# Optimization experiments

Measured on AMD Instinct MI355X. Metric: run time of the kernel, lower is better.

Reference implementation:

```python
import jax, jax.numpy as jnp
import numpy as np

B, L, D = 64, 1024, 64  # (batch*heads, seq_len, head_dim)


def setup_inputs() -> dict:
    key = jax.random.key(0)
    kq, kk, kv = jax.random.split(key, 3)
    q = jax.random.normal(kq, (B, L, D), dtype=jnp.float32)
    k = jax.random.normal(kk, (B, L, D), dtype=jnp.float32)
    v = jax.random.normal(kv, (B, L, D), dtype=jnp.float32)
    scale = jnp.float32(1.0 / np.sqrt(D))  # standard 1/sqrt(d_head)
    return {"q": q, "k": k, "v": v, "scale": scale}


def reference(q, k, v, scale):
    # attention = bmm(q, k^T) * scale  -> [B, L, L]
    attention = jnp.einsum("bqd,bkd->bqk", q, k) * scale
    # softmax over dim=2 (keys); dropout p=0.0 is identity
    attention = jax.nn.softmax(attention, axis=2)
    # context = bmm(attention, v) -> [B, L, D]
    context = jnp.einsum("bqk,bkd->bqd", attention, v)
    return (context, attention)
```

## Files before the change

### kernel.cpp

```cpp
#include <hip/hip_runtime.h>
#include <hip/hip_bf16.h>

typedef __bf16 bf16x8 __attribute__((ext_vector_type(8)));
typedef __bf16 bf16x4 __attribute__((ext_vector_type(4)));
typedef float  f32x4  __attribute__((ext_vector_type(4)));

#define NB 64
#define LL 1024
#define DD 64
#define PB 40

#define WS_VT_OFF 0
#define WS_KB_OFF ((size_t)8 * 1024 * 1024)
#define WS_NEED   ((size_t)16 * 1024 * 1024)

#if __has_builtin(__builtin_amdgcn_exp2f)
#define EXP2(x) __builtin_amdgcn_exp2f(x)
#else
#define EXP2(x) exp2f(x)
#endif

__global__ __launch_bounds__(256)
void preconvert_kv(const float* __restrict__ k, const float* __restrict__ v,
                   __bf16* __restrict__ kbf, __bf16* __restrict__ vt) {
  const int blk = blockIdx.x, tid = threadIdx.x;
  if (blk < NB * (LL / 64)) {
    const int b = blk >> 4, t = blk & 15;
    __shared__ float tile[64][65];
    const float* src = v + ((size_t)b * LL + t * 64) * DD;
    for (int i = tid; i < 64 * 16; i += 256) {
      const int row = i >> 4, c4 = (i & 15) * 4;
      f32x4 x = *(const f32x4*)(src + row * DD + c4);
      tile[row][c4 + 0] = x[0]; tile[row][c4 + 1] = x[1];
      tile[row][c4 + 2] = x[2]; tile[row][c4 + 3] = x[3];
    }
    __syncthreads();
    __bf16* dst = vt + (size_t)b * DD * LL + t * 64;
    for (int i = tid; i < 64 * 8; i += 256) {
      const int d = i >> 3, k8 = (i & 7) * 8;
      bf16x8 o;
      #pragma unroll
      for (int j = 0; j < 8; ++j) o[j] = (__bf16)tile[k8 + j][d];
      *(bf16x8*)(dst + (size_t)d * LL + k8) = o;
    }
  } else {
    const size_t base = ((size_t)(blk - 1024) * 256 + tid) * 8;
    const f32x4* s = (const f32x4*)(k + base);
    f32x4 x0 = s[0], x1 = s[1];
    bf16x8 o;
    #pragma unroll
    for (int j = 0; j < 4; ++j) { o[j] = (__bf16)x0[j]; o[4 + j] = (__bf16)x1[j]; }
    *(bf16x8*)(kbf + base) = o;
  }
}

__global__ __launch_bounds__(256, 4)
void sdpa_quarter(const float* __restrict__ q, const __bf16* __restrict__ kbf,
                  const __bf16* __restrict__ vt, const float* __restrict__ scale_p,
                  float* __restrict__ out) {
  __shared__ __bf16 Kq[256 * 64];
  __shared__ __bf16 Pw[4 * 16 * PB];

  const int tid  = threadIdx.x;
  const int lane = tid & 63;
  const int w    = tid >> 6;
  const int l15  = lane & 15;
  const int lg   = lane >> 4;

  int bid = blockIdx.x;
  bid = (bid & 7) * 128 + (bid >> 3);
  const int b     = bid >> 4;
  const int qrow0 = (bid & 15) * 64 + w * 16;

  const float scale2 = scale_p[0] * 1.4426950408889634f;
  const __bf16* kb = kbf + (size_t)b * LL * DD;
  const __bf16* vb = vt  + (size_t)b * DD * LL;
  float* ctxb  = out + ((size_t)b * LL + qrow0) * DD;
  float* attnb = out + (size_t)NB * LL * DD + (size_t)b * LL * LL
               + (size_t)qrow0 * LL;

  bf16x8 aq[2];
  {
    const float* qrow = q + ((size_t)b * LL + qrow0 + l15) * DD;
    #pragma unroll
    for (int s = 0; s < 2; ++s) {
      const f32x4* p4 = (const f32x4*)(qrow + s * 32 + lg * 8);
      f32x4 x0 = p4[0], x1 = p4[1];
      #pragma unroll
      for (int j = 0; j < 4; ++j) {
        aq[s][j]     = (__bf16)(x0[j] * scale2);
        aq[s][4 + j] = (__bf16)(x1[j] * scale2);
      }
    }
  }

  const int xsw = (l15 & 7) * 8;
  __bf16* prow = Pw + (w * 16 + l15) * PB;

  float ls = 0.f;
  for (int qt = 0; qt < 4; ++qt) {
    __syncthreads();
    #pragma unroll
    for (int it = 0; it < 8; ++it) {
      const int c = it * 256 + tid;
      const int row = c >> 3, slot = c & 7;
      bf16x8 t = *(const bf16x8*)(kb + (size_t)(qt * 256 + row) * 64 + slot * 8);
      *(bf16x8*)(Kq + row * 64 + ((slot * 8) ^ ((row & 7) * 8))) = t;
    }
    __syncthreads();
    for (int kt = 0; kt < 8; ++kt) {
      bf16x8 bk[2][2];
      #pragma unroll
      for (int f = 0; f < 2; ++f)
        #pragma unroll
        for (int s = 0; s < 2; ++s)
          bk[f][s] = *(const bf16x8*)(Kq + (kt * 32 + f * 16 + l15) * 64
                                         + ((s * 32 + lg * 8) ^ xsw));
      f32x4 sacc[2] = {{0.f,0.f,0.f,0.f},{0.f,0.f,0.f,0.f}};
      #pragma unroll
      for (int s = 0; s < 2; ++s)
        #pragma unroll
        for (int f = 0; f < 2; ++f)
          sacc[f] = __builtin_amdgcn_mfma_f32_16x16x32_bf16(bk[f][s], aq[s], sacc[f], 0, 0, 0);
      #pragma unroll
      for (int f = 0; f < 2; ++f)
        #pragma unroll
        for (int r = 0; r < 4; ++r)
          ls += EXP2(sacc[f][r]);
    }
  }
  ls += __shfl_xor(ls, 16, 64);
  ls += __shfl_xor(ls, 32, 64);
  const float rl = 1.0f / ls;

  f32x4 cacc[4];
  #pragma unroll
  for (int g = 0; g < 4; ++g) cacc[g] = (f32x4){0.f, 0.f, 0.f, 0.f};

  for (int qt = 0; qt < 4; ++qt) {
    __syncthreads();
    #pragma unroll
    for (int it = 0; it < 8; ++it) {
      const int c = it * 256 + tid;
      const int row = c >> 3, slot = c & 7;
      bf16x8 t = *(const bf16x8*)(kb + (size_t)(qt * 256 + row) * 64 + slot * 8);
      *(bf16x8*)(Kq + row * 64 + ((slot * 8) ^ ((row & 7) * 8))) = t;
    }
    __syncthreads();

    for (int kt = 0; kt < 8; ++kt) {
      bf16x8 bv[4];
      #pragma unroll
      for (int g = 0; g < 4; ++g)
        bv[g] = *(const bf16x8*)(vb + (size_t)(g * 16 + l15) * LL
                                    + qt * 256 + kt * 32 + lg * 8);

      bf16x8 bk[2][2];
      #pragma unroll
      for (int f = 0; f < 2; ++f)
        #pragma unroll
        for (int s = 0; s < 2; ++s)
          bk[f][s] = *(const bf16x8*)(Kq + (kt * 32 + f * 16 + l15) * 64
                                         + ((s * 32 + lg * 8) ^ xsw));

      f32x4 sacc[2] = {{0.f,0.f,0.f,0.f},{0.f,0.f,0.f,0.f}};
      #pragma unroll
      for (int s = 0; s < 2; ++s)
        #pragma unroll
        for (int f = 0; f < 2; ++f)
          sacc[f] = __builtin_amdgcn_mfma_f32_16x16x32_bf16(bk[f][s], aq[s], sacc[f], 0, 0, 0);

      f32x4 pv[2];
      #pragma unroll
      for (int f = 0; f < 2; ++f)
        #pragma unroll
        for (int r = 0; r < 4; ++r)
          pv[f][r] = EXP2(sacc[f][r]) * rl;

      float* arow = attnb + (size_t)l15 * LL + qt * 256 + kt * 32 + lg * 4;
      *(f32x4*)(arow)      = pv[0];
      *(f32x4*)(arow + 16) = pv[1];

      #pragma unroll
      for (int f = 0; f < 2; ++f) {
        bf16x4 pb;
        #pragma unroll
        for (int r = 0; r < 4; ++r) pb[r] = (__bf16)pv[f][r];
        *(bf16x4*)(prow + f * 16 + lg * 4) = pb;
      }
      bf16x8 pa = *(const bf16x8*)(prow + lg * 8);
      #pragma unroll
      for (int g = 0; g < 4; ++g)
        cacc[g] = __builtin_amdgcn_mfma_f32_16x16x32_bf16(pa, bv[g], cacc[g], 0, 0, 0);
    }
  }

  #pragma unroll
  for (int g = 0; g < 4; ++g)
    #pragma unroll
    for (int r = 0; r < 4; ++r)
      ctxb[(size_t)(lg * 4 + r) * DD + g * 16 + l15] = cacc[g][r];
}

#define BQ 64
#define BK 32
#define KSTRIDE 72
#define VSTRIDE 40
#define PSTRIDE 48

__global__ __launch_bounds__(256, 4)
void sdpa_fallback(const float* __restrict__ q, const float* __restrict__ k,
                   const float* __restrict__ v, const float* __restrict__ scale_p,
                   float* __restrict__ out) {
  const int tid  = threadIdx.x;
  const int lane = tid & 63;
  const int w    = tid >> 6;
  int bid = blockIdx.x;
  bid = (bid & 7) * 128 + (bid >> 3);
  const int b    = bid >> 4;
  const int qblk = (bid & 15) * BQ;

  __shared__ __bf16 Ks[BK * KSTRIDE];
  __shared__ __bf16 Vs[DD * VSTRIDE];
  __shared__ __bf16 Pp[4][16 * PSTRIDE];

  const float scale = scale_p[0];
  const float* qb = q + ((size_t)b * LL + qblk) * DD;
  const float* kb = k + (size_t)b * LL * DD;
  const float* vb = v + (size_t)b * LL * DD;
  float* ctx  = out + ((size_t)b * LL + qblk) * DD;
  float* attn = out + (size_t)NB * LL * DD + (size_t)b * LL * LL + (size_t)qblk * LL;

  const int l15 = lane & 15;
  const int lg  = lane >> 4;
  const int dchunk = lg * 8;

  bf16x8 aq[2];
  {
    const float* qrow = qb + (size_t)(w * 16 + l15) * DD;
    #pragma unroll
    for (int s = 0; s < 2; ++s) {
      const f32x4* p4 = (const f32x4*)(qrow + s * 32 + dchunk);
      f32x4 x0 = p4[0], x1 = p4[1];
      #pragma unroll
      for (int j = 0; j < 4; ++j) {
        aq[s][j]     = (__bf16)(x0[j] * scale);
        aq[s][4 + j] = (__bf16)(x1[j] * scale);
      }
    }
  }

  const int srow = tid >> 3;
  const int sd0  = (tid & 7) * 8;

  float lpart[4] = {0.f, 0.f, 0.f, 0.f};
  for (int kt = 0; kt < LL / BK; ++kt) {
    __syncthreads();
    {
      const f32x4* src = (const f32x4*)(kb + (size_t)(kt * BK + srow) * DD + sd0);
      f32x4 x0 = src[0], x1 = src[1];
      bf16x8 t;
      #pragma unroll
      for (int j = 0; j < 4; ++j) { t[j] = (__bf16)x0[j]; t[4 + j] = (__bf16)x1[j]; }
      *(bf16x8*)&Ks[srow * KSTRIDE + sd0] = t;
    }
    __syncthreads();
    f32x4 sacc[2] = {{0.f,0.f,0.f,0.f},{0.f,0.f,0.f,0.f}};
    #pragma unroll
    for (int s = 0; s < 2; ++s)
      #pragma unroll
      for (int f = 0; f < 2; ++f) {
        bf16x8 bk = *(const bf16x8*)&Ks[(f * 16 + l15) * KSTRIDE + s * 32 + dchunk];
        sacc[f] = __builtin_amdgcn_mfma_f32_16x16x32_bf16(aq[s], bk, sacc[f], 0, 0, 0);
      }
    #pragma unroll
    for (int f = 0; f < 2; ++f)
      #pragma unroll
      for (int r = 0; r < 4; ++r)
        lpart[r] += __expf(sacc[f][r]);
  }
  #pragma unroll
  for (int m = 1; m < 16; m <<= 1)
    #pragma unroll
    for (int r = 0; r < 4; ++r)
      lpart[r] += __shfl_xor(lpart[r], m, 64);
  float rl[4];
  #pragma unroll
  for (int r = 0; r < 4; ++r) rl[r] = 1.0f / lpart[r];

  f32x4 cacc[4] = {{0.f,0.f,0.f,0.f},{0.f,0.f,0.f,0.f},
                   {0.f,0.f,0.f,0.f},{0.f,0.f,0.f,0.f}};
  for (int kt = 0; kt < LL / BK; ++kt) {
    __syncthreads();
    {
      const f32x4* src = (const f32x4*)(kb + (size_t)(kt * BK + srow) * DD + sd0);
      f32x4 x0 = src[0], x1 = src[1];
      bf16x8 t;
      #pragma unroll
      for (int j = 0; j < 4; ++j) { t[j] = (__bf16)x0[j]; t[4 + j] = (__bf16)x1[j]; }
      *(bf16x8*)&Ks[srow * KSTRIDE + sd0] = t;
      const f32x4* vsrc = (const f32x4*)(vb + (size_t)(kt * BK + srow) * DD + sd0);
      f32x4 y0 = vsrc[0], y1 = vsrc[1];
      #pragma unroll
      for (int j = 0; j < 4; ++j) {
        Vs[(sd0 + j)     * VSTRIDE + srow] = (__bf16)y0[j];
        Vs[(sd0 + 4 + j) * VSTRIDE + srow] = (__bf16)y1[j];
      }
    }
    __syncthreads();
    f32x4 sacc[2] = {{0.f,0.f,0.f,0.f},{0.f,0.f,0.f,0.f}};
    #pragma unroll
    for (int s = 0; s < 2; ++s)
      #pragma unroll
      for (int f = 0; f < 2; ++f) {
        bf16x8 bk = *(const bf16x8*)&Ks[(f * 16 + l15) * KSTRIDE + s * 32 + dchunk];
        sacc[f] = __builtin_amdgcn_mfma_f32_16x16x32_bf16(aq[s], bk, sacc[f], 0, 0, 0);
      }
    #pragma unroll
    for (int f = 0; f < 2; ++f)
      #pragma unroll
      for (int r = 0; r < 4; ++r) {
        const int row = lg * 4 + r;
        float p = __expf(sacc[f][r]) * rl[r];
        attn[(size_t)(w * 16 + row) * LL + (kt * BK + f * 16 + l15)] = p;
        Pp[w][row * PSTRIDE + f * 16 + l15] = (__bf16)p;
      }
    bf16x8 pa = *(const bf16x8*)&Pp[w][l15 * PSTRIDE + lg * 8];
    #pragma unroll
    for (int g = 0; g < 4; ++g) {
      bf16x8 bv = *(const bf16x8*)&Vs[(g * 16 + l15) * VSTRIDE + lg * 8];
      cacc[g] = __builtin_amdgcn_mfma_f32_16x16x32_bf16(pa, bv, cacc[g], 0, 0, 0);
    }
  }
  #pragma unroll
  for (int g = 0; g < 4; ++g)
    #pragma unroll
    for (int r = 0; r < 4; ++r)
      ctx[(size_t)(w * 16 + lg * 4 + r) * DD + g * 16 + l15] = cacc[g][r];
}

extern "C" void kernel_launch(void* const* d_in, const int* in_sizes, int n_in,
                              void* d_out, int out_size, void* d_ws, size_t ws_size,
                              hipStream_t stream) {
  const float* q = (const float*)d_in[0];
  const float* k = (const float*)d_in[1];
  const float* v = (const float*)d_in[2];
  const float* s = (const float*)d_in[3];
  float* out = (float*)d_out;

  if (ws_size >= WS_NEED) {
    __bf16* vt  = (__bf16*)((char*)d_ws + WS_VT_OFF);
    __bf16* kbf = (__bf16*)((char*)d_ws + WS_KB_OFF);
    preconvert_kv<<<dim3(3072), dim3(256), 0, stream>>>(k, v, kbf, vt);
    sdpa_quarter<<<dim3(1024), dim3(256), 0, stream>>>(q, kbf, vt, s, out);
  } else {
    sdpa_fallback<<<dim3(NB * (LL / 64)), dim3(256), 0, stream>>>(q, k, v, s, out);
  }
}
```

Baseline: 113.0 us.

## Restructure attention into 256-row panel blocks with LDS-staged coalesced attention writes

Result: slower. 124.7 us (+10.4%).

```diff
diff --git a/kernel.cpp b/kernel.cpp
--- a/kernel.cpp
+++ b/kernel.cpp
@@ -8,7 +8,10 @@
 #define NB 64
 #define LL 1024
 #define DD 64
-#define PB 40
+#define HK 512
+#define PAN 264
+
+#define PANEL_LDS (HK * DD * 2 + 8 * 16 * PAN * 2)
 
 #define WS_VT_OFF 0
 #define WS_KB_OFF ((size_t)8 * 1024 * 1024)
@@ -54,12 +57,13 @@
   }
 }
 
-__global__ __launch_bounds__(256, 4)
-void sdpa_quarter(const float* __restrict__ q, const __bf16* __restrict__ kbf,
-                  const __bf16* __restrict__ vt, const float* __restrict__ scale_p,
-                  float* __restrict__ out) {
-  __shared__ __bf16 Kq[256 * 64];
-  __shared__ __bf16 Pw[4 * 16 * PB];
+__global__ __launch_bounds__(512, 1)
+void sdpa_panel(const float* __restrict__ q, const __bf16* __restrict__ kbf,
+                const __bf16* __restrict__ vt, const float* __restrict__ scale_p,
+                float* __restrict__ out) {
+  extern __shared__ char smem[];
+  __bf16* Klds = (__bf16*)smem;
+  __bf16* Pan  = (__bf16*)(smem + HK * DD * 2);
 
   const int tid  = threadIdx.x;
   const int lane = tid & 63;
@@ -68,9 +72,9 @@
   const int lg   = lane >> 4;
 
   int bid = blockIdx.x;
-  bid = (bid & 7) * 128 + (bid >> 3);
-  const int b     = bid >> 4;
-  const int qrow0 = (bid & 15) * 64 + w * 16;
+  bid = (bid & 7) * 32 + (bid >> 3);
+  const int b     = bid >> 2;
+  const int qrow0 = (bid & 3) * 256 + w * 32;
 
   const float scale2 = scale_p[0] * 1.4426950408889634f;
   const __bf16* kb = kbf + (size_t)b * LL * DD;
@@ -79,127 +83,149 @@
   float* attnb = out + (size_t)NB * LL * DD + (size_t)b * LL * LL
                + (size_t)qrow0 * LL;
 
-  bf16x8 aq[2];
-  {
-    const float* qrow = q + ((size_t)b * LL + qrow0 + l15) * DD;
+  bf16x8 aq[2][2];
+  #pragma unroll
+  for (int u = 0; u < 2; ++u) {
+    const float* qrow = q + ((size_t)b * LL + qrow0 + u * 16 + l15) * DD;
     #pragma unroll
     for (int s = 0; s < 2; ++s) {
       const f32x4* p4 = (const f32x4*)(qrow + s * 32 + lg * 8);
       f32x4 x0 = p4[0], x1 = p4[1];
       #pragma unroll
       for (int j = 0; j < 4; ++j) {
-        aq[s][j]     = (__bf16)(x0[j] * scale2);
-        aq[s][4 + j] = (__bf16)(x1[j] * scale2);
+        aq[u][s][j]     = (__bf16)(x0[j] * scale2);
+        aq[u][s][4 + j] = (__bf16)(x1[j] * scale2);
       }
     }
   }
 
   const int xsw = (l15 & 7) * 8;
-  __bf16* prow = Pw + (w * 16 + l15) * PB;
-
-  float ls = 0.f;
-  for (int qt = 0; qt < 4; ++qt) {
+  __bf16* pw = Pan + (size_t)w * 16 * PAN;
+
+  float ls[2] = {0.f, 0.f};
+  for (int h = 0; h < 2; ++h) {
     __syncthreads();
     #pragma unroll
     for (int it = 0; it < 8; ++it) {
-      const int c = it * 256 + tid;
+      const int c = it * 512 + tid;
       const int row = c >> 3, slot = c & 7;
-      bf16x8 t = *(const bf16x8*)(kb + (size_t)(qt * 256 + row) * 64 + slot * 8);
-      *(bf16x8*)(Kq + row * 64 + ((slot * 8) ^ ((row & 7) * 8))) = t;
-    }
-    __syncthreads();
-    for (int kt = 0; kt < 8; ++kt) {
+      bf16x8 t = *(const bf16x8*)(kb + (size_t)(h * HK + row) * 64 + slot * 8);
+      *(bf16x8*)(Klds + row * 64 + ((slot * 8) ^ ((row & 7) * 8))) = t;
+    }
+    __syncthreads();
+    for (int kt = 0; kt < HK / 32; ++kt) {
       bf16x8 bk[2][2];
       #pragma unroll
       for (int f = 0; f < 2; ++f)
         #pragma unroll
         for (int s = 0; s < 2; ++s)
-          bk[f][s] = *(const bf16x8*)(Kq + (kt * 32 + f * 16 + l15) * 64
-                                         + ((s * 32 + lg * 8) ^ xsw));
-      f32x4 sacc[2] = {{0.f,0.f,0.f,0.f},{0.f,0.f,0.f,0.f}};
-      #pragma unroll
-      for (int s = 0; s < 2; ++s)
+          bk[f][s] = *(const bf16x8*)(Klds + (kt * 32 + f * 16 + l15) * 64
+                                           + ((s * 32 + lg * 8) ^ xsw));
+      #pragma unroll
+      for (int u = 0; u < 2; ++u) {
+        f32x4 sacc[2] = {{0.f,0.f,0.f,0.f},{0.f,0.f,0.f,0.f}};
+        #pragma unroll
+        for (int s = 0; s < 2; ++s)
+          #pragma unroll
+          for (int f = 0; f < 2; ++f)
+            sacc[f] = __builtin_amdgcn_mfma_f32_16x16x32_bf16(bk[f][s], aq[u][s], sacc[f], 0, 0, 0);
         #pragma unroll
         for (int f = 0; f < 2; ++f)
-          sacc[f] = __builtin_amdgcn_mfma_f32_16x16x32_bf16(bk[f][s], aq[s], sacc[f], 0, 0, 0);
-      #pragma unroll
-      for (int f = 0; f < 2; ++f)
+          #pragma unroll
+          for (int r = 0; r < 4; ++r)
+            ls[u] += EXP2(sacc[f][r]);
+      }
+    }
+  }
+  #pragma unroll
+  for (int u = 0; u < 2; ++u) {
+    ls[u] += __shfl_xor(ls[u], 16, 64);
+    ls[u] += __shfl_xor(ls[u], 32, 64);
+  }
+  const float rl[2] = {1.0f / ls[0], 1.0f / ls[1]};
+
+  f32x4 cacc[2][4];
+  #pragma unroll
+  for (int u = 0; u < 2; ++u)
+    #pragma unroll
+    for (int g = 0; g < 4; ++g)
+      cacc[u][g] = (f32x4){0.f, 0.f, 0.f, 0.f};
+
+  for (int h = 0; h < 2; ++h) {
+    __syncthreads();
+    #pragma unroll
+    for (int it = 0; it < 8; ++it) {
+      const int c = it * 512 + tid;
+      const int row = c >> 3, slot = c & 7;
+      bf16x8 t = *(const bf16x8*)(kb + (size_t)(h * HK + row) * 64 + slot * 8);
+      *(bf16x8*)(Klds + row * 64 + ((slot * 8) ^ ((row & 7) * 8))) = t;
+    }
+    __syncthreads();
+
+    for (int pc = 0; pc < 2; ++pc) {
+      #pragma unroll
+      for (int u = 0; u < 2; ++u) {
+        for (int kt8 = 0; kt8 < 8; ++kt8) {
+          const int kt = pc * 8 + kt8;
+
+          bf16x8 bv[4];
+          #pragma unroll
+          for (int g = 0; g < 4; ++g)
+            bv[g] = *(const bf16x8*)(vb + (size_t)(g * 16 + l15) * LL
+                                        + h * HK + kt * 32 + lg * 8);
+
+          bf16x8 bk[2][2];
+          #pragma unroll
+          for (int f = 0; f < 2; ++f)
+            #pragma unroll
+            for (int s = 0; s < 2; ++s)
+              bk[f][s] = *(const bf16x8*)(Klds + (kt * 32 + f * 16 + l15) * 64
+                                               + ((s * 32 + lg * 8) ^ xsw));
+
+          f32x4 sacc[2] = {{0.f,0.f,0.f,0.f},{0.f,0.f,0.f,0.f}};
+          #pragma unroll
+          for (int s = 0; s < 2; ++s)
+            #pragma unroll
+            for (int f = 0; f < 2; ++f)
+              sacc[f] = __builtin_amdgcn_mfma_f32_16x16x32_bf16(bk[f][s], aq[u][s], sacc[f], 0, 0, 0);
+
+          #pragma unroll
+          for (int f = 0; f < 2; ++f) {
+            bf16x4 pb;
+            #pragma unroll
+            for (int r = 0; r < 4; ++r)
+              pb[r] = (__bf16)(EXP2(sacc[f][r]) * rl[u]);
+            *(bf16x4*)(pw + l15 * PAN + kt8 * 32 + f * 16 + lg * 4) = pb;
+          }
+
+          bf16x8 pa = *(const bf16x8*)(pw + l15 * PAN + kt8 * 32 + lg * 8);
+          #pragma unroll
+          for (int g = 0; g < 4; ++g)
+            cacc[u][g] = __builtin_amdgcn_mfma_f32_16x16x32_bf16(pa, bv[g], cacc[u][g], 0, 0, 0);
+        }
+
+        float* ab = attnb + (size_t)(u * 16) * LL + h * HK + pc * 256;
         #pragma unroll
-        for (int r = 0; r < 4; ++r)
-          ls += EXP2(sacc[f][r]);
-    }
-  }
-  ls += __shfl_xor(ls, 16, 64);
-  ls += __shfl_xor(ls, 32, 64);
-  const float rl = 1.0f / ls;
-
-  f32x4 cacc[4];
-  #pragma unroll
-  for (int g = 0; g < 4; ++g) cacc[g] = (f32x4){0.f, 0.f, 0.f, 0.f};
-
-  for (int qt = 0; qt < 4; ++qt) {
-    __syncthreads();
-    #pragma unroll
-    for (int it = 0; it < 8; ++it) {
-      const int c = it * 256 + tid;
-      const int row = c >> 3, slot = c & 7;
-      bf16x8 t = *(const bf16x8*)(kb + (size_t)(qt * 256 + row) * 64 + slot * 8);
-      *(bf16x8*)(Kq + row * 64 + ((slot * 8) ^ ((row & 7) * 8))) = t;
-    }
-    __syncthreads();
-
-    for (int kt = 0; kt < 8; ++kt) {
-      bf16x8 bv[4];
-      #pragma unroll
-      for (int g = 0; g < 4; ++g)
-        bv[g] = *(const bf16x8*)(vb + (size_t)(g * 16 + l15) * LL
-                                    + qt * 256 + kt * 32 + lg * 8);
-
-      bf16x8 bk[2][2];
-      #pragma unroll
-      for (int f = 0; f < 2; ++f)
-        #pragma unroll
-        for (int s = 0; s < 2; ++s)
-          bk[f][s] = *(const bf16x8*)(Kq + (kt * 32 + f * 16 + l15) * 64
-                                         + ((s * 32 + lg * 8) ^ xsw));
-
-      f32x4 sacc[2] = {{0.f,0.f,0.f,0.f},{0.f,0.f,0.f,0.f}};
-      #pragma unroll
-      for (int s = 0; s < 2; ++s)
-        #pragma unroll
-        for (int f = 0; f < 2; ++f)
-          sacc[f] = __builtin_amdgcn_mfma_f32_16x16x32_bf16(bk[f][s], aq[s], sacc[f], 0, 0, 0);
-
-      f32x4 pv[2];
-      #pragma unroll
-      for (int f = 0; f < 2; ++f)
-        #pragma unroll
-        for (int r = 0; r < 4; ++r)
-          pv[f][r] = EXP2(sacc[f][r]) * rl;
-
-      float* arow = attnb + (size_t)l15 * LL + qt * 256 + kt * 32 + lg * 4;
-      *(f32x4*)(arow)      = pv[0];
-      *(f32x4*)(arow + 16) = pv[1];
-
-      #pragma unroll
-      for (int f = 0; f < 2; ++f) {
-        bf16x4 pb;
-        #pragma unroll
-        for (int r = 0; r < 4; ++r) pb[r] = (__bf16)pv[f][r];
-        *(bf16x4*)(prow + f * 16 + lg * 4) = pb;
-      }
-      bf16x8 pa = *(const bf16x8*)(prow + lg * 8);
-      #pragma unroll
-      for (int g = 0; g < 4; ++g)
-        cacc[g] = __builtin_amdgcn_mfma_f32_16x16x32_bf16(pa, bv[g], cacc[g], 0, 0, 0);
-    }
-  }
-
-  #pragma unroll
-  for (int g = 0; g < 4; ++g)
-    #pragma unroll
-    for (int r = 0; r < 4; ++r)
-      ctxb[(size_t)(lg * 4 + r) * DD + g * 16 + l15] = cacc[g][r];
+        for (int r = 0; r < 16; ++r) {
+          const uint2 rw = *(const uint2*)(pw + r * PAN + lane * 4);
+          f32x4 o;
+          o[0] = __uint_as_float(rw.x << 16);
+          o[1] = __uint_as_float(rw.x & 0xffff0000u);
+          o[2] = __uint_as_float(rw.y << 16);
+          o[3] = __uint_as_float(rw.y & 0xffff0000u);
+          *(f32x4*)(ab + (size_t)r * LL + lane * 4) = o;
+        }
+      }
+    }
+  }
+
+  #pragma unroll
+  for (int u = 0; u < 2; ++u)
+    #pragma unroll
+    for (int g = 0; g < 4; ++g)
+      #pragma unroll
+      for (int r = 0; r < 4; ++r)
+        ctxb[(size_t)(u * 16 + lg * 4 + r) * DD + g * 16 + l15] = cacc[u][g][r];
 }
 
 #define BQ 64
@@ -352,7 +378,9 @@
     __bf16* vt  = (__bf16*)((char*)d_ws + WS_VT_OFF);
     __bf16* kbf = (__bf16*)((char*)d_ws + WS_KB_OFF);
     preconvert_kv<<<dim3(3072), dim3(256), 0, stream>>>(k, v, kbf, vt);
-    sdpa_quarter<<<dim3(1024), dim3(256), 0, stream>>>(q, kbf, vt, s, out);
+    (void)hipFuncSetAttribute((const void*)sdpa_panel,
+                              hipFuncAttributeMaxDynamicSharedMemorySize, PANEL_LDS);
+    sdpa_panel<<<dim3(256), dim3(512), PANEL_LDS, stream>>>(q, kbf, vt, s, out);
   } else {
     sdpa_fallback<<<dim3(NB * (LL / 64)), dim3(256), 0, stream>>>(q, k, v, s, out);
   }
```
